# Performance work log

Measured on AMD Instinct MI355X. Metric: run time of the kernel, lower is better.

The kernel has to match this reference:

```python
import jax, jax.numpy as jnp
import numpy as np

HEAD_DIM = 128
SCALE = 1.0 / np.sqrt(HEAD_DIM).astype(np.float32)


def setup_inputs() -> dict:
    key = jax.random.key(0)
    kq, kk, kv = jax.random.split(key, 3)
    B, S, H, KVH, D = 2, 2048, 32, 8, HEAD_DIM
    q = jax.random.normal(kq, (B, S, H, D), dtype=jnp.float32)
    k = jax.random.normal(kk, (B, S, KVH, D), dtype=jnp.float32)
    v = jax.random.normal(kv, (B, S, KVH, D), dtype=jnp.float32)
    return {"q": q, "k": k, "v": v}


def reference(q, k, v):
    # q: [B,S,H,D]; k,v: [B,S,KVH,D]
    B, S, H, D = q.shape
    kvh = k.shape[2]
    if kvh != H:
        rep = H // kvh
        # repeat_interleave along head dim (GQA -> MHA expansion)
        k = jnp.repeat(k, rep, axis=2)
        v = jnp.repeat(v, rep, axis=2)
    # scores: [B,H,S,S]
    scores = jnp.einsum("bqhd,bkhd->bhqk", q, k) * SCALE
    causal_mask = jnp.triu(jnp.ones((S, S), dtype=bool), k=1)
    scores = jnp.where(causal_mask, -jnp.inf, scores)
    attn = jax.nn.softmax(scores, axis=-1)
    # output back to [B,S,H,D]
    out = jnp.einsum("bhqk,bkhd->bqhd", attn, v)
    return out
```

## Files before the change

kernel.cpp:

```cpp
#include <hip/hip_runtime.h>
#include <hip/hip_bf16.h>
#include <stdint.h>

#define B_    2
#define S_    2048
#define H_    32
#define KVH_  8
#define D_    128
#define NBLK  512
#define NTOT_ 68

typedef __bf16 bf16x8 __attribute__((ext_vector_type(8)));
typedef unsigned short u16x8 __attribute__((ext_vector_type(8)));
typedef unsigned int u32x4 __attribute__((ext_vector_type(4)));
typedef float f32x16 __attribute__((ext_vector_type(16)));

__device__ constexpr float SCALE_LOG2E = 0.08838834764831845f * 1.4426950408889634f;

__device__ __forceinline__ unsigned short f2bf(float f) {
    unsigned int u = __builtin_bit_cast(unsigned int, f);
    u = (u + 0x7FFFu + ((u >> 16) & 1u)) >> 16;
    return (unsigned short)u;
}

__device__ __forceinline__ unsigned int cvt_pk_bf16(float lo, float hi) {
    unsigned int r;
    asm("v_cvt_pk_bf16_f32 %0, %1, %2" : "=v"(r) : "v"(lo), "v"(hi));
    return r;
}

__device__ __forceinline__ void gload16(const unsigned short* gsrc, unsigned short* ldst) {
    __builtin_amdgcn_global_load_lds(
        (const __attribute__((address_space(1))) unsigned int*)gsrc,
        (__attribute__((address_space(3))) unsigned int*)ldst,
        16, 0, 0);
}

__global__ __launch_bounds__(256) void prepass(const float* __restrict__ k,
                                               const float* __restrict__ v,
                                               unsigned short* __restrict__ kbuf,
                                               unsigned short* __restrict__ vbuf) {
    if (blockIdx.x < 2048) {
        int tid = blockIdx.x * 256 + threadIdx.x;
        int l   = tid & 63;
        int ch  = (tid >> 6) & 7;
        int kt  = (tid >> 9) & 63;
        int kvh = (tid >> 15) & 7;
        int b   = (tid >> 18) & 1;
        int s   = kt * 32 + (l & 31);
        int d0  = ch * 16 + (l >> 5) * 8;
        const float* src = k + (((size_t)b * S_ + s) * KVH_ + kvh) * D_ + d0;
        float4 x = ((const float4*)src)[0];
        float4 y = ((const float4*)src)[1];
        u16x8 o;
        o[0] = f2bf(x.x); o[1] = f2bf(x.y); o[2] = f2bf(x.z); o[3] = f2bf(x.w);
        o[4] = f2bf(y.x); o[5] = f2bf(y.y); o[6] = f2bf(y.z); o[7] = f2bf(y.w);
        *(u16x8*)(kbuf + ((size_t)(((b * KVH_ + kvh) * 64 + kt) * 8 + ch) * 512 + l * 8)) = o;
    } else {
        __shared__ float tile[64][132];
        int bid = blockIdx.x - 2048;
        int u   = bid & 31;
        int kvh = (bid >> 5) & 7;
        int b   = bid >> 8;
        int t   = threadIdx.x;

        int s  = t >> 2;
        int cb = (t & 3) * 32;
        const float* src = v + (((size_t)b * S_ + u * 64 + s) * KVH_ + kvh) * D_ + cb;
        #pragma unroll
        for (int i = 0; i < 8; ++i) {
            float4 x = ((const float4*)src)[i];
            tile[s][cb + 4 * i + 0] = x.x; tile[s][cb + 4 * i + 1] = x.y;
            tile[s][cb + 4 * i + 2] = x.z; tile[s][cb + 4 * i + 3] = x.w;
        }
        __syncthreads();

        #pragma unroll
        for (int i = 0; i < 4; ++i) {
            int slot = t + 256 * i;
            int ci = slot >> 6;
            int l  = slot & 63;
            int kk = ci >> 2, dt = ci & 3;
            int h2 = l >> 5;
            u16x8 o;
            #pragma unroll
            for (int j = 0; j < 8; ++j)
                o[j] = f2bf(tile[kk * 16 + h2 * 8 + j][dt * 32 + (l & 31)]);
            *(u16x8*)(vbuf + ((size_t)(((b * KVH_ + kvh) * 32 + u) * 16 + ci) * 512 + l * 8)) = o;
        }
    }
}

__global__ __launch_bounds__(256, 2)
void attn_fwd(const float* __restrict__ q,
              const unsigned short* __restrict__ kbuf,
              const unsigned short* __restrict__ vbuf,
              float* __restrict__ out)
{
    int pid = blockIdx.x;
    int lid = (pid & 7) * (NBLK / 8) + (pid >> 3);
    int p   = lid & 7;
    int bh  = lid >> 3;
    int b   = bh >> 5, h = bh & 31, kvh = h >> 2;
    const int qtA = 15 - p;
    const int NTA = 4 * qtA + 4;
    const int qtB = p;

    const int tid = threadIdx.x, wave = tid >> 6, lane = tid & 63;
    const int cw = wave;
    const int c32 = lane & 31, hi = lane >> 5;

    __shared__ __align__(16) unsigned short ldsK[2][4096];
    __shared__ __align__(16) unsigned short ldsV[2][4096];

    const unsigned short* kfb = kbuf + (size_t)(b * KVH_ + kvh) * (S_ * D_);
    const unsigned short* vfb = vbuf + (size_t)(b * KVH_ + kvh) * (S_ * D_);

    auto kvt = [&](int u) { return (u < NTA) ? u : (u - NTA); };
    auto stageK = [&](int u) {
        const unsigned short* ks = kfb + (size_t)kvt(u) * 4096;
        unsigned short* ld = &ldsK[u & 1][0];
        #pragma unroll
        for (int i = 0; i < 2; ++i) {
            int seg = wave * 2 + i;
            gload16(ks + seg * 512 + lane * 8, ld + seg * 512);
        }
    };
    auto stageV = [&](int u) {
        const unsigned short* vs = vfb + (size_t)kvt(u) * 4096;
        unsigned short* ld = &ldsV[u & 1][0];
        #pragma unroll
        for (int i = 0; i < 2; ++i) {
            int seg = wave * 2 + i;
            gload16(vs + seg * 512 + lane * 8, ld + seg * 512);
        }
    };

    stageK(0);
    asm volatile("s_waitcnt vmcnt(0)" ::: "memory");
    __builtin_amdgcn_s_barrier();
    asm volatile("" ::: "memory");

    auto run_tile = [&](int qt, int u0, int NT) {
        const int q0w = qt * 128 + cw * 32;

        bf16x8 qf[8];
        {
            const float* qp = q + ((size_t)b * S_ + q0w + c32) * (H_ * D_) + h * D_ + hi * 8;
            #pragma unroll
            for (int ch = 0; ch < 8; ++ch) {
                float4 a  = ((const float4*)(qp + ch * 16))[0];
                float4 bb = ((const float4*)(qp + ch * 16))[1];
                u16x8 tt;
                tt[0] = f2bf(a.x * SCALE_LOG2E);  tt[1] = f2bf(a.y * SCALE_LOG2E);
                tt[2] = f2bf(a.z * SCALE_LOG2E);  tt[3] = f2bf(a.w * SCALE_LOG2E);
                tt[4] = f2bf(bb.x * SCALE_LOG2E); tt[5] = f2bf(bb.y * SCALE_LOG2E);
                tt[6] = f2bf(bb.z * SCALE_LOG2E); tt[7] = f2bf(bb.w * SCALE_LOG2E);
                qf[ch] = __builtin_bit_cast(bf16x8, tt);
            }
        }

        f32x16 acc[4];
        #pragma unroll
        for (int dt = 0; dt < 4; ++dt)
            #pragma unroll
            for (int i = 0; i < 16; ++i) acc[dt][i] = 0.f;
        float lsum = 0.f;

        u32x4 pfA[2], pfB[2];

        auto body = [&](int u, int it, u32x4 (&pfW)[2], u32x4 (&pfR)[2], int ODD) {
            if (u + 1 < NTOT_) stageK(u + 1);
            stageV(u);
            const int k0 = it * 32;
            const bool act  = (k0 <= q0w + 31);
            const bool pact = (it > 0) && (k0 - 32 <= q0w + 31);
            f32x16 sv;

            if (act) {
                #pragma unroll
                for (int i = 0; i < 16; ++i) sv[i] = 0.f;
                __builtin_amdgcn_s_setprio(1);
                #pragma unroll
                for (int ch = 0; ch < 8; ++ch) {
                    bf16x8 kf = *(const bf16x8*)&ldsK[ODD][ch * 512 + lane * 8];
                    sv = __builtin_amdgcn_mfma_f32_32x32x16_bf16(kf, qf[ch], sv, 0, 0, 0);
                }
                __builtin_amdgcn_s_setprio(0);
            }

            if (pact) {
                __builtin_amdgcn_s_setprio(1);
                #pragma unroll
                for (int kk = 0; kk < 2; ++kk) {
                    bf16x8 pb = __builtin_bit_cast(bf16x8, pfR[kk]);
                    #pragma unroll
                    for (int dt = 0; dt < 4; ++dt) {
                        bf16x8 vf = *(const bf16x8*)&ldsV[ODD ^ 1][(kk * 4 + dt) * 512 + lane * 8];
                        acc[dt] = __builtin_amdgcn_mfma_f32_32x32x16_bf16(vf, pb, acc[dt], 0, 0, 0);
                    }
                }
                __builtin_amdgcn_s_setprio(0);
            }

            if (act) {
                if (k0 + 31 > q0w) {
                    #pragma unroll
                    for (int r = 0; r < 16; ++r) {
                        int key = k0 + (r & 3) + 8 * (r >> 2) + 4 * hi;
                        if (key > q0w + c32) sv[r] = -INFINITY;
                    }
                }

                float pp[16];
                #pragma unroll
                for (int r = 0; r < 16; ++r) pp[r] = exp2f(sv[r]);
                float s0 = (pp[0] + pp[1]) + (pp[2] + pp[3]);
                float s1 = (pp[4] + pp[5]) + (pp[6] + pp[7]);
                float s2 = (pp[8] + pp[9]) + (pp[10] + pp[11]);
                float s3 = (pp[12] + pp[13]) + (pp[14] + pp[15]);
                lsum += (s0 + s1) + (s2 + s3);

                #pragma unroll
                for (int kap = 0; kap < 2; ++kap) {
                    int base = kap * 8;
                    unsigned int U0 = cvt_pk_bf16(pp[base + 0], pp[base + 1]);
                    unsigned int U1 = cvt_pk_bf16(pp[base + 2], pp[base + 3]);
                    unsigned int V0 = cvt_pk_bf16(pp[base + 4], pp[base + 5]);
                    unsigned int V1 = cvt_pk_bf16(pp[base + 6], pp[base + 7]);
                    asm volatile("v_permlane32_swap_b32 %0, %1" : "+v"(U0), "+v"(V0));
                    asm volatile("v_permlane32_swap_b32 %0, %1" : "+v"(U1), "+v"(V1));
                    u32x4 W;
                    W[0] = U0;
                    W[1] = U1;
                    W[2] = V0;
                    W[3] = V1;
                    pfW[kap] = W;
                }
            }

            asm volatile("s_waitcnt vmcnt(0)" ::: "memory");
            __builtin_amdgcn_s_barrier();
            asm volatile("" ::: "memory");
        };

        for (int it = 0; it < NT; it += 2) {
            body(u0 + it,     it,     pfA, pfB, 0);
            body(u0 + it + 1, it + 1, pfB, pfA, 1);
        }

        if (cw == 3) {
            #pragma unroll
            for (int kk = 0; kk < 2; ++kk) {
                bf16x8 pb = __builtin_bit_cast(bf16x8, pfB[kk]);
                #pragma unroll
                for (int dt = 0; dt < 4; ++dt) {
                    bf16x8 vf = *(const bf16x8*)&ldsV[1][(kk * 4 + dt) * 512 + lane * 8];
                    acc[dt] = __builtin_amdgcn_mfma_f32_32x32x16_bf16(vf, pb, acc[dt], 0, 0, 0);
                }
            }
        }

        lsum += __shfl_xor(lsum, 32);
        float linv = 1.0f / lsum;
        float* ob = out + ((size_t)b * S_ + q0w + c32) * (H_ * D_) + h * D_;
        #pragma unroll
        for (int dt = 0; dt < 4; ++dt)
            #pragma unroll
            for (int rq = 0; rq < 4; ++rq) {
                float4 o;
                o.x = acc[dt][4 * rq + 0] * linv;
                o.y = acc[dt][4 * rq + 1] * linv;
                o.z = acc[dt][4 * rq + 2] * linv;
                o.w = acc[dt][4 * rq + 3] * linv;
                *(float4*)(ob + dt * 32 + rq * 8 + hi * 4) = o;
            }
    };

    run_tile(qtA, 0, NTA);
    run_tile(qtB, NTA, NTOT_ - NTA);
}

extern "C" void kernel_launch(void* const* d_in, const int* in_sizes, int n_in,
                              void* d_out, int out_size, void* d_ws, size_t ws_size,
                              hipStream_t stream) {
    const float* q = (const float*)d_in[0];
    const float* k = (const float*)d_in[1];
    const float* v = (const float*)d_in[2];
    float* out = (float*)d_out;

    unsigned short* kbuf = (unsigned short*)d_ws;
    unsigned short* vbuf = kbuf + (size_t)B_ * KVH_ * S_ * D_;

    prepass<<<2560, 256, 0, stream>>>(k, v, kbuf, vbuf);
    attn_fwd<<<NBLK, 256, 0, stream>>>(q, kbuf, vbuf, out);
}
```

Before: 118.4 us.

## Replace LDS-staged K/V pipeline with per-wave direct register loads and independent loops

Drops the shared-memory double buffers, global_load_lds staging and per-iteration block barriers. Each wave now loads its own K and V fragments straight from global memory into registers, prefetching the next tile, and runs only the causal tiles it needs. The second tile reverses the wave-to-slice mapping to balance work across waves. This removes barrier stalls and skipped-tile waiting, but each wave re-reads K/V from global/L2 instead of sharing one LDS copy. The higher register use from holding kf/vf arrays may lower occupancy, since the two-blocks-per-CU launch bound is also dropped.

Result: slower. 133.2 us (+12.5%).

```diff
diff --git a/kernel.cpp b/kernel.cpp
--- a/kernel.cpp
+++ b/kernel.cpp
@@ -8,7 +8,6 @@
 #define KVH_  8
 #define D_    128
 #define NBLK  512
-#define NTOT_ 68
 
 typedef __bf16 bf16x8 __attribute__((ext_vector_type(8)));
 typedef unsigned short u16x8 __attribute__((ext_vector_type(8)));
@@ -27,13 +26,6 @@
     unsigned int r;
     asm("v_cvt_pk_bf16_f32 %0, %1, %2" : "=v"(r) : "v"(lo), "v"(hi));
     return r;
-}
-
-__device__ __forceinline__ void gload16(const unsigned short* gsrc, unsigned short* ldst) {
-    __builtin_amdgcn_global_load_lds(
-        (const __attribute__((address_space(1))) unsigned int*)gsrc,
-        (__attribute__((address_space(3))) unsigned int*)ldst,
-        16, 0, 0);
 }
 
 __global__ __launch_bounds__(256) void prepass(const float* __restrict__ k,
@@ -91,7 +83,7 @@
     }
 }
 
-__global__ __launch_bounds__(256, 2)
+__global__ __launch_bounds__(256)
 void attn_fwd(const float* __restrict__ q,
               const unsigned short* __restrict__ kbuf,
               const unsigned short* __restrict__ vbuf,
@@ -103,46 +95,17 @@
     int bh  = lid >> 3;
     int b   = bh >> 5, h = bh & 31, kvh = h >> 2;
     const int qtA = 15 - p;
-    const int NTA = 4 * qtA + 4;
     const int qtB = p;
 
     const int tid = threadIdx.x, wave = tid >> 6, lane = tid & 63;
-    const int cw = wave;
     const int c32 = lane & 31, hi = lane >> 5;
 
-    __shared__ __align__(16) unsigned short ldsK[2][4096];
-    __shared__ __align__(16) unsigned short ldsV[2][4096];
-
-    const unsigned short* kfb = kbuf + (size_t)(b * KVH_ + kvh) * (S_ * D_);
-    const unsigned short* vfb = vbuf + (size_t)(b * KVH_ + kvh) * (S_ * D_);
-
-    auto kvt = [&](int u) { return (u < NTA) ? u : (u - NTA); };
-    auto stageK = [&](int u) {
-        const unsigned short* ks = kfb + (size_t)kvt(u) * 4096;
-        unsigned short* ld = &ldsK[u & 1][0];
-        #pragma unroll
-        for (int i = 0; i < 2; ++i) {
-            int seg = wave * 2 + i;
-            gload16(ks + seg * 512 + lane * 8, ld + seg * 512);
-        }
-    };
-    auto stageV = [&](int u) {
-        const unsigned short* vs = vfb + (size_t)kvt(u) * 4096;
-        unsigned short* ld = &ldsV[u & 1][0];
-        #pragma unroll
-        for (int i = 0; i < 2; ++i) {
-            int seg = wave * 2 + i;
-            gload16(vs + seg * 512 + lane * 8, ld + seg * 512);
-        }
-    };
-
-    stageK(0);
-    asm volatile("s_waitcnt vmcnt(0)" ::: "memory");
-    __builtin_amdgcn_s_barrier();
-    asm volatile("" ::: "memory");
-
-    auto run_tile = [&](int qt, int u0, int NT) {
-        const int q0w = qt * 128 + cw * 32;
+    const unsigned short* kfb = kbuf + (size_t)(b * KVH_ + kvh) * (S_ * D_) + lane * 8;
+    const unsigned short* vfb = vbuf + (size_t)(b * KVH_ + kvh) * (S_ * D_) + lane * 8;
+
+    auto run_tile = [&](int qt, int slice) {
+        const int q0w = qt * 128 + slice * 32;
+        const int NT  = (q0w >> 5) + 1;
 
         bf16x8 qf[8];
         {
@@ -167,97 +130,79 @@
             for (int i = 0; i < 16; ++i) acc[dt][i] = 0.f;
         float lsum = 0.f;
 
-        u32x4 pfA[2], pfB[2];
-
-        auto body = [&](int u, int it, u32x4 (&pfW)[2], u32x4 (&pfR)[2], int ODD) {
-            if (u + 1 < NTOT_) stageK(u + 1);
-            stageV(u);
-            const int k0 = it * 32;
-            const bool act  = (k0 <= q0w + 31);
-            const bool pact = (it > 0) && (k0 - 32 <= q0w + 31);
+        bf16x8 kf[8], vf[8];
+        const unsigned short* kp = kfb;
+        const unsigned short* vp = vfb;
+        #pragma unroll
+        for (int ch = 0; ch < 8; ++ch) kf[ch] = *(const bf16x8*)(kp + ch * 512);
+        #pragma unroll
+        for (int ci = 0; ci < 8; ++ci) vf[ci] = *(const bf16x8*)(vp + ci * 512);
+
+        for (int it = 0; it < NT; ++it) {
             f32x16 sv;
-
-            if (act) {
-                #pragma unroll
-                for (int i = 0; i < 16; ++i) sv[i] = 0.f;
-                __builtin_amdgcn_s_setprio(1);
-                #pragma unroll
-                for (int ch = 0; ch < 8; ++ch) {
-                    bf16x8 kf = *(const bf16x8*)&ldsK[ODD][ch * 512 + lane * 8];
-                    sv = __builtin_amdgcn_mfma_f32_32x32x16_bf16(kf, qf[ch], sv, 0, 0, 0);
+            #pragma unroll
+            for (int i = 0; i < 16; ++i) sv[i] = 0.f;
+            __builtin_amdgcn_s_setprio(1);
+            #pragma unroll
+            for (int ch = 0; ch < 8; ++ch)
+                sv = __builtin_amdgcn_mfma_f32_32x32x16_bf16(kf[ch], qf[ch], sv, 0, 0, 0);
+            __builtin_amdgcn_s_setprio(0);
+
+            kp += 4096;
+            if (it + 1 < NT) {
+                #pragma unroll
+                for (int ch = 0; ch < 8; ++ch) kf[ch] = *(const bf16x8*)(kp + ch * 512);
+            }
+
+            if (it == NT - 1) {
+                #pragma unroll
+                for (int r = 0; r < 16; ++r) {
+                    int loc = (r & 3) + 8 * (r >> 2) + 4 * hi;
+                    if (loc > c32) sv[r] = -INFINITY;
                 }
-                __builtin_amdgcn_s_setprio(0);
-            }
-
-            if (pact) {
-                __builtin_amdgcn_s_setprio(1);
-                #pragma unroll
-                for (int kk = 0; kk < 2; ++kk) {
-                    bf16x8 pb = __builtin_bit_cast(bf16x8, pfR[kk]);
-                    #pragma unroll
-                    for (int dt = 0; dt < 4; ++dt) {
-                        bf16x8 vf = *(const bf16x8*)&ldsV[ODD ^ 1][(kk * 4 + dt) * 512 + lane * 8];
-                        acc[dt] = __builtin_amdgcn_mfma_f32_32x32x16_bf16(vf, pb, acc[dt], 0, 0, 0);
-                    }
-                }
-                __builtin_amdgcn_s_setprio(0);
-            }
-
-            if (act) {
-                if (k0 + 31 > q0w) {
-                    #pragma unroll
-                    for (int r = 0; r < 16; ++r) {
-                        int key = k0 + (r & 3) + 8 * (r >> 2) + 4 * hi;
-                        if (key > q0w + c32) sv[r] = -INFINITY;
-                    }
-                }
-
-                float pp[16];
-                #pragma unroll
-                for (int r = 0; r < 16; ++r) pp[r] = exp2f(sv[r]);
-                float s0 = (pp[0] + pp[1]) + (pp[2] + pp[3]);
-                float s1 = (pp[4] + pp[5]) + (pp[6] + pp[7]);
-                float s2 = (pp[8] + pp[9]) + (pp[10] + pp[11]);
-                float s3 = (pp[12] + pp[13]) + (pp[14] + pp[15]);
-                lsum += (s0 + s1) + (s2 + s3);
-
-                #pragma unroll
-                for (int kap = 0; kap < 2; ++kap) {
-                    int base = kap * 8;
-                    unsigned int U0 = cvt_pk_bf16(pp[base + 0], pp[base + 1]);
-                    unsigned int U1 = cvt_pk_bf16(pp[base + 2], pp[base + 3]);
-                    unsigned int V0 = cvt_pk_bf16(pp[base + 4], pp[base + 5]);
-                    unsigned int V1 = cvt_pk_bf16(pp[base + 6], pp[base + 7]);
-                    asm volatile("v_permlane32_swap_b32 %0, %1" : "+v"(U0), "+v"(V0));
-                    asm volatile("v_permlane32_swap_b32 %0, %1" : "+v"(U1), "+v"(V1));
-                    u32x4 W;
-                    W[0] = U0;
-                    W[1] = U1;
-                    W[2] = V0;
-                    W[3] = V1;
-                    pfW[kap] = W;
-                }
-            }
-
-            asm volatile("s_waitcnt vmcnt(0)" ::: "memory");
-            __builtin_amdgcn_s_barrier();
-            asm volatile("" ::: "memory");
-        };
-
-        for (int it = 0; it < NT; it += 2) {
-            body(u0 + it,     it,     pfA, pfB, 0);
-            body(u0 + it + 1, it + 1, pfB, pfA, 1);
-        }
-
-        if (cw == 3) {
+            }
+
+            float pp[16];
+            #pragma unroll
+            for (int r = 0; r < 16; ++r) pp[r] = exp2f(sv[r]);
+            float s0 = (pp[0] + pp[1]) + (pp[2] + pp[3]);
+            float s1 = (pp[4] + pp[5]) + (pp[6] + pp[7]);
+            float s2 = (pp[8] + pp[9]) + (pp[10] + pp[11]);
+            float s3 = (pp[12] + pp[13]) + (pp[14] + pp[15]);
+            lsum += (s0 + s1) + (s2 + s3);
+
+            u32x4 pf[2];
+            #pragma unroll
+            for (int kap = 0; kap < 2; ++kap) {
+                int base = kap * 8;
+                unsigned int U0 = cvt_pk_bf16(pp[base + 0], pp[base + 1]);
+                unsigned int U1 = cvt_pk_bf16(pp[base + 2], pp[base + 3]);
+                unsigned int V0 = cvt_pk_bf16(pp[base + 4], pp[base + 5]);
+                unsigned int V1 = cvt_pk_bf16(pp[base + 6], pp[base + 7]);
+                asm volatile("v_permlane32_swap_b32 %0, %1" : "+v"(U0), "+v"(V0));
+                asm volatile("v_permlane32_swap_b32 %0, %1" : "+v"(U1), "+v"(V1));
+                u32x4 W;
+                W[0] = U0;
+                W[1] = U1;
+                W[2] = V0;
+                W[3] = V1;
+                pf[kap] = W;
+            }
+
+            __builtin_amdgcn_s_setprio(1);
             #pragma unroll
             for (int kk = 0; kk < 2; ++kk) {
-                bf16x8 pb = __builtin_bit_cast(bf16x8, pfB[kk]);
-                #pragma unroll
-                for (int dt = 0; dt < 4; ++dt) {
-                    bf16x8 vf = *(const bf16x8*)&ldsV[1][(kk * 4 + dt) * 512 + lane * 8];
-                    acc[dt] = __builtin_amdgcn_mfma_f32_32x32x16_bf16(vf, pb, acc[dt], 0, 0, 0);
-                }
+                bf16x8 pb = __builtin_bit_cast(bf16x8, pf[kk]);
+                #pragma unroll
+                for (int dt = 0; dt < 4; ++dt)
+                    acc[dt] = __builtin_amdgcn_mfma_f32_32x32x16_bf16(vf[kk * 4 + dt], pb, acc[dt], 0, 0, 0);
+            }
+            __builtin_amdgcn_s_setprio(0);
+
+            vp += 4096;
+            if (it + 1 < NT) {
+                #pragma unroll
+                for (int ci = 0; ci < 8; ++ci) vf[ci] = *(const bf16x8*)(vp + ci * 512);
             }
         }
 
@@ -277,8 +222,8 @@
             }
     };
 
-    run_tile(qtA, 0, NTA);
-    run_tile(qtB, NTA, NTOT_ - NTA);
+    run_tile(qtA, wave);
+    run_tile(qtB, 3 - wave);
 }
 
 extern "C" void kernel_launch(void* const* d_in, const int* in_sizes, int n_in,
```
